# Optimization experiments

Measured on AMD Instinct MI355X. Metric: run time of the kernel, lower is better.

The kernel has to match this reference:

```python
import jax, jax.numpy as jnp
import numpy as np

B, T, D = 16, 4096, 256
CODEBOOK_SIZE = 1024
COMMITMENT = 1.0


def setup_inputs() -> dict:
    key = jax.random.key(0)
    kx, kc = jax.random.split(key)
    x = jax.random.normal(kx, (B, T, D), dtype=jnp.float32)
    codebook = jax.random.normal(kc, (CODEBOOK_SIZE, D), dtype=jnp.float32)
    return {"x": x, "codebook": codebook}


def reference(x, codebook):
    # x: [B, T, D] continuous latents; codebook: [K, D]
    flat = x.reshape(-1, x.shape[-1])  # [N, D]
    # does not affect argmin but is kept for faithfulness to torch.cdist-style math)
    x_sq = jnp.sum(flat * flat, axis=1, keepdims=True)            # [N, 1]
    c_sq = jnp.sum(codebook * codebook, axis=1)                   # [K]
    dist = x_sq - 2.0 * (flat @ codebook.T) + c_sq[None, :]       # [N, K]
    indices = jnp.argmin(dist, axis=1)                            # [N] int
    quantized = codebook[indices].reshape(x.shape)                # gather, [B, T, D]
    # commitment loss: encoder pulled toward (stopped) codes
    commit_loss = COMMITMENT * jnp.mean(
        (x - jax.lax.stop_gradient(quantized)) ** 2
    )
    # straight-through estimator
    out = x + jax.lax.stop_gradient(quantized - x)
    return out, indices.reshape(x.shape[:-1]), commit_loss
```

## Files before the change

### kernel.cpp

```cpp
#include <hip/hip_runtime.h>

#define N_TOK 65536
#define DIM   256
#define KCODE 1024

#define NTHREADS 256
#define TM 128
#define TN 128
#define BK 32
#define NCHUNK 8
#define NSTAGE 24

#define REFINE_EPS 0.125f
#define TIE_THETA 1.0e-4

#define WS_CSQ_OFF   16
#define WS_IDX_OFF   2048
#define WS_PAIRS_OFF (WS_IDX_OFF + N_TOK)
#define WS_CBPK_OFF  (WS_PAIRS_OFF + N_TOK * NCHUNK * 4)

typedef float f32x4  __attribute__((ext_vector_type(4)));
typedef short bf16x8 __attribute__((ext_vector_type(8)));
typedef short s16x8  __attribute__((ext_vector_type(8)));

__global__ void zero_loss_kernel(float* ws) {
    if (threadIdx.x == 0) ws[0] = 0.0f;
}

__global__ void rowsq_np_kernel(const float* __restrict__ m,
                                float* __restrict__ out, int rows) {
#pragma clang fp contract(off)
    int row = blockIdx.x * 16 + (threadIdx.x >> 4);
    int l   = threadIdx.x & 15;
    if (row >= rows) return;
    int h = l >> 3;
    int j = l & 7;
    const float* p = m + (size_t)row * DIM + h * 128 + j;
    float v = p[0];
    float r = v * v;
#pragma unroll
    for (int i = 1; i < 16; ++i) {
        float w  = p[i * 8];
        float w2 = w * w;
        r = r + w2;
    }
    float t = r + __shfl_xor(r, 1);
    t = t + __shfl_xor(t, 2);
    t = t + __shfl_xor(t, 4);
    t = t + __shfl_xor(t, 8);
    if (l == 0) out[row] = t;
}

__device__ __forceinline__ void ins2(float d, int idx,
                                     float& d1, int& i1, float& d2, int& i2) {
    if (d < d1 || (d == d1 && idx < i1)) {
        d2 = d1; i2 = i1; d1 = d; i1 = idx;
    } else if ((d < d2 || (d == d2 && idx < i2)) && idx != i1) {
        d2 = d; i2 = idx;
    }
}

__device__ __forceinline__ void f2bf_split(float v, short& hi, short& lo) {
    unsigned u = __float_as_uint(v);
    unsigned r = (u + 0x7fffu + ((u >> 16) & 1u)) >> 16;
    hi = (short)r;
    float hf = __uint_as_float(r << 16);
    float lf = v - hf;
    unsigned u2 = __float_as_uint(lf);
    unsigned r2 = (u2 + 0x7fffu + ((u2 >> 16) & 1u)) >> 16;
    lo = (short)r2;
}

__global__ void pack_tiles_kernel(const float* __restrict__ src,
                                  unsigned short* __restrict__ dst,
                                  int total) {
    int tid = blockIdx.x * blockDim.x + threadIdx.x;
    if (tid >= total) return;
    int s   = tid & 3;
    int r   = (tid >> 2) & 127;
    int kc  = (tid >> 9) & 7;
    int g   = tid >> 12;
    int oct = s ^ ((r >> 1) & 3);

    const float4* xr = reinterpret_cast<const float4*>(
        src + ((size_t)(g * 128 + r)) * DIM + kc * 32 + oct * 8);
    float4 v0 = xr[0];
    float4 v1 = xr[1];

    float f[8] = {v0.x, v0.y, v0.z, v0.w, v1.x, v1.y, v1.z, v1.w};
    s16x8 hv, lv;
#pragma unroll
    for (int i = 0; i < 8; ++i) {
        short h, l;
        f2bf_split(f[i], h, l);
        hv[i] = h; lv[i] = l;
    }
    size_t base_hi = (((size_t)(g * 16 + kc) * 128 + r) << 5) + s * 8;
    size_t base_lo = (((size_t)(g * 16 + 8 + kc) * 128 + r) << 5) + s * 8;
    *reinterpret_cast<s16x8*>(dst + base_hi) = hv;
    *reinterpret_cast<s16x8*>(dst + base_lo) = lv;
}

__device__ __forceinline__ void gload_lds16(const unsigned short* g, unsigned short* lds) {
    __builtin_amdgcn_global_load_lds(
        (const __attribute__((address_space(1))) unsigned int*)g,
        (__attribute__((address_space(3))) unsigned int*)lds, 16, 0, 0);
}

__launch_bounds__(NTHREADS, 5)
__global__ void vq_main_kernel(const unsigned short* __restrict__ xpk,
                               const unsigned short* __restrict__ cbpk,
                               const float* __restrict__ csq,
                               float4* __restrict__ pairs) {
    __shared__ __align__(16) unsigned short shbuf[2][2 * TM * BK];

    const int tid  = threadIdx.x;
    const int w    = tid >> 6;
    const int wy   = w >> 1;
    const int wx   = w & 1;
    const int lane = tid & 63;
    const int lm   = lane & 15;
    const int q    = lane >> 4;

    const int bx     = blockIdx.x;
    const int jj     = bx >> 3;
    const int grp    = (bx & 7) + ((jj >> 3) << 3);
    const int cchunk = jj & 7;
    const int tok0   = grp * TM;
    const int code0  = cchunk * TN;

    float cs_reg[4];
#pragma unroll
    for (int ni = 0; ni < 4; ++ni)
        cs_reg[ni] = csq[code0 + wx * 64 + ni * 16 + lm];

    f32x4 acc[4][4];
#pragma unroll
    for (int mi = 0; mi < 4; ++mi)
#pragma unroll
        for (int ni = 0; ni < 4; ++ni)
            acc[mi][ni] = (f32x4){0.f, 0.f, 0.f, 0.f};

    int offA[4], offB[4];
#pragma unroll
    for (int mi = 0; mi < 4; ++mi) {
        int r = wy * 64 + mi * 16 + lm;
        offA[mi] = r * BK + ((q ^ ((r >> 1) & 3)) * 8);
    }
#pragma unroll
    for (int ni = 0; ni < 4; ++ni) {
        int r = wx * 64 + ni * 16 + lm;
        offB[ni] = TM * BK + r * BK + ((q ^ ((r >> 1) & 3)) * 8);
    }

    const int lsrc = w * 1024 + lane * 8;
    auto stage = [&](int p, int s) {
        const int seg = s >> 3;
        const int kc  = s & 7;
        const int pa  = (seg == 2) ? 8 : 0;
        const int pb  = (seg == 1) ? 8 : 0;
        const unsigned short* ga = xpk  + (((size_t)(grp    * 16 + pa + kc)) << 12) + lsrc;
        const unsigned short* gb = cbpk + (((size_t)(cchunk * 16 + pb + kc)) << 12) + lsrc;
        unsigned short* At = &shbuf[p][w * 1024];
        unsigned short* Bt = &shbuf[p][TM * BK + w * 1024];
        gload_lds16(ga,       At);
        gload_lds16(ga + 512, At + 512);
        gload_lds16(gb,       Bt);
        gload_lds16(gb + 512, Bt + 512);
    };

    stage(0, 0);
    __syncthreads();

    int p = 0;
#pragma unroll 1
    for (int s = 0; s < NSTAGE; ++s) {
        if (s < NSTAGE - 1) stage(p ^ 1, s + 1);

        const unsigned short* buf = &shbuf[p][0];
        bf16x8 af[4], bf[4];
#pragma unroll
        for (int mi = 0; mi < 4; ++mi)
            af[mi] = *reinterpret_cast<const bf16x8*>(buf + offA[mi]);
#pragma unroll
        for (int ni = 0; ni < 4; ++ni)
            bf[ni] = *reinterpret_cast<const bf16x8*>(buf + offB[ni]);
#pragma unroll
        for (int mi = 0; mi < 4; ++mi)
#pragma unroll
            for (int ni = 0; ni < 4; ++ni)
                acc[mi][ni] = __builtin_amdgcn_mfma_f32_16x16x32_bf16(
                    af[mi], bf[ni], acc[mi][ni], 0, 0, 0);

        __syncthreads();
        p ^= 1;
    }

    float4 (*pairs_sh)[2] = reinterpret_cast<float4(*)[2]>(&shbuf[0][0]);

#pragma unroll
    for (int mi = 0; mi < 4; ++mi) {
#pragma unroll
        for (int r = 0; r < 4; ++r) {
            int row_local = wy * 64 + mi * 16 + q * 4 + r;
            float l1 = 3.4e38f, l2 = 3.4e38f;
            int   j1 = 0x7fffffff, j2 = 0x7fffffff;
#pragma unroll
            for (int ni = 0; ni < 4; ++ni) {
                float d = cs_reg[ni] - 2.0f * acc[mi][ni][r];
                ins2(d, code0 + wx * 64 + ni * 16 + lm, l1, j1, l2, j2);
            }
#pragma unroll
            for (int m = 1; m < 16; m <<= 1) {
                float o1 = __shfl_xor(l1, m);
                int   p1 = __shfl_xor(j1, m);
                float o2 = __shfl_xor(l2, m);
                int   p2 = __shfl_xor(j2, m);
                ins2(o1, p1, l1, j1, l2, j2);
                ins2(o2, p2, l1, j1, l2, j2);
            }
            if (lm == 0) {
                float4 pr;
                pr.x = l1; pr.y = l2;
                pr.z = __int_as_float(j1); pr.w = __int_as_float(j2);
                pairs_sh[row_local][wx] = pr;
            }
        }
    }
    __syncthreads();
    if (tid < TM) {
        float4 pa = pairs_sh[tid][0];
        float4 pb = pairs_sh[tid][1];
        float d1 = pa.x, d2 = pa.y;
        int   i1 = __float_as_int(pa.z), i2 = __float_as_int(pa.w);
        ins2(pb.x, __float_as_int(pb.z), d1, i1, d2, i2);
        ins2(pb.y, __float_as_int(pb.w), d1, i1, d2, i2);
        float4 pr;
        pr.x = d1; pr.y = d2;
        pr.z = __int_as_float(i1); pr.w = __int_as_float(i2);
        pairs[(size_t)(tok0 + tid) * NCHUNK + cchunk] = pr;
    }
}

__global__ void merge_refine_kernel(const float* __restrict__ x,
                                    const float* __restrict__ cb,
                                    const float4* __restrict__ pairs,
                                    int* __restrict__ idx_out) {
    int t = blockIdx.x * 256 + threadIdx.x;
    if (t >= N_TOK) return;
    float4 p0 = pairs[(size_t)t * NCHUNK];
    float d1 = p0.x, d2 = p0.y;
    int   i1 = __float_as_int(p0.z), i2 = __float_as_int(p0.w);
#pragma unroll
    for (int c = 1; c < NCHUNK; ++c) {
        float4 p = pairs[(size_t)t * NCHUNK + c];
        ins2(p.x, __float_as_int(p.z), d1, i1, d2, i2);
        ins2(p.y, __float_as_int(p.w), d1, i1, d2, i2);
    }

    int pick = i1;
    if (d2 - d1 < REFINE_EPS) {
        const float* xr = x + (size_t)t * DIM;
        const float* c1 = cb + (size_t)i1 * DIM;
        const float* c2 = cb + (size_t)i2 * DIM;
        double sA = 0.0, dA = 0.0, sB = 0.0, dB = 0.0;
        for (int k = 0; k < DIM; ++k) {
            double xv = (double)xr[k];
            double a  = (double)c1[k];
            double b  = (double)c2[k];
            sA += a * a; dA += xv * a;
            sB += b * b; dB += xv * b;
        }
        double DA  = sA - 2.0 * dA;
        double DB  = sB - 2.0 * dB;
        double gap = DB - DA;
        if (gap > TIE_THETA)       pick = i1;
        else if (gap < -TIE_THETA) pick = i2;
        else                       pick = (i1 < i2) ? i1 : i2;
    }
    idx_out[t] = pick;
}

__launch_bounds__(NTHREADS)
__global__ void output_kernel(const float* __restrict__ x,
                              const float* __restrict__ cb,
                              const int* __restrict__ idx,
                              float* __restrict__ out_q,
                              float* __restrict__ out_idx,
                              float* __restrict__ loss_ws) {
    __shared__ int   sh_idx[TM];
    __shared__ float wsum[4];
    const int tid  = threadIdx.x;
    const int tok0 = blockIdx.x * TM;

    if (tid < TM) sh_idx[tid] = idx[tok0 + tid];
    __syncthreads();

    float lsum = 0.0f;
    for (int t = 0; t < TM; ++t) {
        int code = sh_idx[t];
        float qv = cb[(size_t)code * DIM + tid];
        float xv = x[(size_t)(tok0 + t) * DIM + tid];
        out_q[(size_t)(tok0 + t) * DIM + tid] = xv + (qv - xv);
        float df = xv - qv;
        lsum = fmaf(df, df, lsum);
    }
    if (tid < TM) out_idx[tok0 + tid] = (float)sh_idx[tid];

#pragma unroll
    for (int off = 1; off < 64; off <<= 1) lsum += __shfl_xor(lsum, off);
    if ((tid & 63) == 0) wsum[tid >> 6] = lsum;
    __syncthreads();
    if (tid == 0) atomicAdd(loss_ws, (wsum[0] + wsum[1]) + (wsum[2] + wsum[3]));
}

__global__ void finalize_kernel(const float* ws, float* out_loss) {
    if (threadIdx.x == 0) out_loss[0] = ws[0] * (1.0f / 16777216.0f);
}

extern "C" void kernel_launch(void* const* d_in, const int* in_sizes, int n_in,
                              void* d_out, int out_size, void* d_ws, size_t ws_size,
                              hipStream_t stream) {
    const float* x  = (const float*)d_in[0];
    const float* cb = (const float*)d_in[1];

    float* out      = (float*)d_out;
    float* out_q    = out;
    float* out_idx  = out + (size_t)N_TOK * DIM;
    float* out_loss = out_idx + N_TOK;

    float*  ws    = (float*)d_ws;
    float*  csq   = ws + WS_CSQ_OFF;
    int*    idx   = (int*)(ws + WS_IDX_OFF);
    float4* pairs = (float4*)(ws + WS_PAIRS_OFF);
    unsigned short* cbpk = (unsigned short*)(ws + WS_CBPK_OFF);
    unsigned short* xpk  = (unsigned short*)out_q;

    zero_loss_kernel<<<1, 64, 0, stream>>>(ws);
    rowsq_np_kernel<<<KCODE / 16, 256, 0, stream>>>(cb, csq, KCODE);
    pack_tiles_kernel<<<(N_TOK * 32) / 256, 256, 0, stream>>>(x, xpk, N_TOK * 32);
    pack_tiles_kernel<<<(KCODE * 32) / 256, 256, 0, stream>>>(cb, cbpk, KCODE * 32);
    vq_main_kernel<<<(N_TOK / TM) * NCHUNK, NTHREADS, 0, stream>>>(xpk, cbpk, csq, pairs);
    merge_refine_kernel<<<N_TOK / 256, 256, 0, stream>>>(x, cb, pairs, idx);
    output_kernel<<<N_TOK / TM, NTHREADS, 0, stream>>>(x, cb, idx, out_q, out_idx, ws);
    finalize_kernel<<<1, 64, 0, stream>>>(ws, out_loss);
}
```

Measured before the change: 803.3 us.

## Triple-buffer GEMM loads, fuse merge into output kernel, drop zero kernel

The main distance kernel now keeps three LDS buffers with two stages in flight, using an explicit vmcnt wait plus barrier instead of __syncthreads, and raises MFMA priority with setprio. The merge/refine step is folded into the output kernel, and the pairs layout is transposed to chunk-major so the merge reads are coalesced. The loss-zeroing kernel is merged into the row-norm kernel. These changes cut launch count and global round trips and aim to hide load latency, at the cost of more LDS per block and lower declared occupancy (launch bound 3 instead of 5).

New measurement: 816.4 us. About the same (+1.6%).

```diff
diff --git a/kernel.cpp b/kernel.cpp
--- a/kernel.cpp
+++ b/kernel.cpp
@@ -10,6 +10,7 @@
 #define BK 32
 #define NCHUNK 8
 #define NSTAGE 24
+#define OTM 128
 
 #define REFINE_EPS 0.125f
 #define TIE_THETA 1.0e-4
@@ -23,13 +24,11 @@
 typedef short bf16x8 __attribute__((ext_vector_type(8)));
 typedef short s16x8  __attribute__((ext_vector_type(8)));
 
-__global__ void zero_loss_kernel(float* ws) {
-    if (threadIdx.x == 0) ws[0] = 0.0f;
-}
-
 __global__ void rowsq_np_kernel(const float* __restrict__ m,
-                                float* __restrict__ out, int rows) {
+                                float* __restrict__ out,
+                                float* __restrict__ loss_ws, int rows) {
 #pragma clang fp contract(off)
+    if (blockIdx.x == 0 && threadIdx.x == 0) loss_ws[0] = 0.0f;
     int row = blockIdx.x * 16 + (threadIdx.x >> 4);
     int l   = threadIdx.x & 15;
     if (row >= rows) return;
@@ -107,12 +106,13 @@
         (__attribute__((address_space(3))) unsigned int*)lds, 16, 0, 0);
 }
 
-__launch_bounds__(NTHREADS, 5)
+__launch_bounds__(NTHREADS, 3)
 __global__ void vq_main_kernel(const unsigned short* __restrict__ xpk,
                                const unsigned short* __restrict__ cbpk,
                                const float* __restrict__ csq,
                                float4* __restrict__ pairs) {
-    __shared__ __align__(16) unsigned short shbuf[2][2 * TM * BK];
+    __shared__ __align__(16) unsigned short shbuf[3][2 * TM * BK];
+    __shared__ float4 pairs_sh[TM][2];
 
     const int tid  = threadIdx.x;
     const int w    = tid >> 6;
@@ -170,14 +170,21 @@
     };
 
     stage(0, 0);
-    __syncthreads();
-
-    int p = 0;
+    stage(1, 1);
+
+    int pc = 0;
 #pragma unroll 1
-    for (int s = 0; s < NSTAGE; ++s) {
-        if (s < NSTAGE - 1) stage(p ^ 1, s + 1);
-
-        const unsigned short* buf = &shbuf[p][0];
+    for (int s = 0; s < NSTAGE - 1; ++s) {
+        asm volatile("s_waitcnt vmcnt(4)" ::: "memory");
+        __builtin_amdgcn_s_barrier();
+        __builtin_amdgcn_sched_barrier(0);
+
+        if (s + 2 < NSTAGE) {
+            int pn = pc + 2; if (pn >= 3) pn -= 3;
+            stage(pn, s + 2);
+        }
+
+        const unsigned short* buf = &shbuf[pc][0];
         bf16x8 af[4], bf[4];
 #pragma unroll
         for (int mi = 0; mi < 4; ++mi)
@@ -185,18 +192,40 @@
 #pragma unroll
         for (int ni = 0; ni < 4; ++ni)
             bf[ni] = *reinterpret_cast<const bf16x8*>(buf + offB[ni]);
+
+        __builtin_amdgcn_s_setprio(1);
 #pragma unroll
         for (int mi = 0; mi < 4; ++mi)
 #pragma unroll
             for (int ni = 0; ni < 4; ++ni)
                 acc[mi][ni] = __builtin_amdgcn_mfma_f32_16x16x32_bf16(
                     af[mi], bf[ni], acc[mi][ni], 0, 0, 0);
-
-        __syncthreads();
-        p ^= 1;
-    }
-
-    float4 (*pairs_sh)[2] = reinterpret_cast<float4(*)[2]>(&shbuf[0][0]);
+        __builtin_amdgcn_s_setprio(0);
+
+        pc = (pc == 2) ? 0 : pc + 1;
+    }
+
+    asm volatile("s_waitcnt vmcnt(0)" ::: "memory");
+    __builtin_amdgcn_s_barrier();
+    __builtin_amdgcn_sched_barrier(0);
+    {
+        const unsigned short* buf = &shbuf[pc][0];
+        bf16x8 af[4], bf[4];
+#pragma unroll
+        for (int mi = 0; mi < 4; ++mi)
+            af[mi] = *reinterpret_cast<const bf16x8*>(buf + offA[mi]);
+#pragma unroll
+        for (int ni = 0; ni < 4; ++ni)
+            bf[ni] = *reinterpret_cast<const bf16x8*>(buf + offB[ni]);
+        __builtin_amdgcn_s_setprio(1);
+#pragma unroll
+        for (int mi = 0; mi < 4; ++mi)
+#pragma unroll
+            for (int ni = 0; ni < 4; ++ni)
+                acc[mi][ni] = __builtin_amdgcn_mfma_f32_16x16x32_bf16(
+                    af[mi], bf[ni], acc[mi][ni], 0, 0, 0);
+        __builtin_amdgcn_s_setprio(0);
+    }
 
 #pragma unroll
     for (int mi = 0; mi < 4; ++mi) {
@@ -238,66 +267,61 @@
         float4 pr;
         pr.x = d1; pr.y = d2;
         pr.z = __int_as_float(i1); pr.w = __int_as_float(i2);
-        pairs[(size_t)(tok0 + tid) * NCHUNK + cchunk] = pr;
-    }
-}
-
-__global__ void merge_refine_kernel(const float* __restrict__ x,
+        pairs[(size_t)cchunk * N_TOK + tok0 + tid] = pr;
+    }
+}
+
+__launch_bounds__(256)
+__global__ void merge_output_kernel(const float* __restrict__ x,
                                     const float* __restrict__ cb,
                                     const float4* __restrict__ pairs,
-                                    int* __restrict__ idx_out) {
-    int t = blockIdx.x * 256 + threadIdx.x;
-    if (t >= N_TOK) return;
-    float4 p0 = pairs[(size_t)t * NCHUNK];
-    float d1 = p0.x, d2 = p0.y;
-    int   i1 = __float_as_int(p0.z), i2 = __float_as_int(p0.w);
-#pragma unroll
-    for (int c = 1; c < NCHUNK; ++c) {
-        float4 p = pairs[(size_t)t * NCHUNK + c];
-        ins2(p.x, __float_as_int(p.z), d1, i1, d2, i2);
-        ins2(p.y, __float_as_int(p.w), d1, i1, d2, i2);
-    }
-
-    int pick = i1;
-    if (d2 - d1 < REFINE_EPS) {
-        const float* xr = x + (size_t)t * DIM;
-        const float* c1 = cb + (size_t)i1 * DIM;
-        const float* c2 = cb + (size_t)i2 * DIM;
-        double sA = 0.0, dA = 0.0, sB = 0.0, dB = 0.0;
-        for (int k = 0; k < DIM; ++k) {
-            double xv = (double)xr[k];
-            double a  = (double)c1[k];
-            double b  = (double)c2[k];
-            sA += a * a; dA += xv * a;
-            sB += b * b; dB += xv * b;
-        }
-        double DA  = sA - 2.0 * dA;
-        double DB  = sB - 2.0 * dB;
-        double gap = DB - DA;
-        if (gap > TIE_THETA)       pick = i1;
-        else if (gap < -TIE_THETA) pick = i2;
-        else                       pick = (i1 < i2) ? i1 : i2;
-    }
-    idx_out[t] = pick;
-}
-
-__launch_bounds__(NTHREADS)
-__global__ void output_kernel(const float* __restrict__ x,
-                              const float* __restrict__ cb,
-                              const int* __restrict__ idx,
-                              float* __restrict__ out_q,
-                              float* __restrict__ out_idx,
-                              float* __restrict__ loss_ws) {
-    __shared__ int   sh_idx[TM];
+                                    float* __restrict__ out_q,
+                                    float* __restrict__ out_idx,
+                                    float* __restrict__ loss_ws) {
+    __shared__ int   sh_idx[OTM];
     __shared__ float wsum[4];
     const int tid  = threadIdx.x;
-    const int tok0 = blockIdx.x * TM;
-
-    if (tid < TM) sh_idx[tid] = idx[tok0 + tid];
+    const int tok0 = blockIdx.x * OTM;
+
+    if (tid < OTM) {
+        const int t = tok0 + tid;
+        float4 p0 = pairs[t];
+        float d1 = p0.x, d2 = p0.y;
+        int   i1 = __float_as_int(p0.z), i2 = __float_as_int(p0.w);
+#pragma unroll
+        for (int c = 1; c < NCHUNK; ++c) {
+            float4 p = pairs[(size_t)c * N_TOK + t];
+            ins2(p.x, __float_as_int(p.z), d1, i1, d2, i2);
+            ins2(p.y, __float_as_int(p.w), d1, i1, d2, i2);
+        }
+
+        int pick = i1;
+        if (d2 - d1 < REFINE_EPS) {
+            const float* xr = x + (size_t)t * DIM;
+            const float* c1 = cb + (size_t)i1 * DIM;
+            const float* c2 = cb + (size_t)i2 * DIM;
+            double sA = 0.0, dA = 0.0, sB = 0.0, dB = 0.0;
+            for (int k = 0; k < DIM; ++k) {
+                double xv = (double)xr[k];
+                double a  = (double)c1[k];
+                double b  = (double)c2[k];
+                sA += a * a; dA += xv * a;
+                sB += b * b; dB += xv * b;
+            }
+            double DA  = sA - 2.0 * dA;
+            double DB  = sB - 2.0 * dB;
+            double gap = DB - DA;
+            if (gap > TIE_THETA)       pick = i1;
+            else if (gap < -TIE_THETA) pick = i2;
+            else                       pick = (i1 < i2) ? i1 : i2;
+        }
+        sh_idx[tid] = pick;
+        out_idx[t]  = (float)pick;
+    }
     __syncthreads();
 
     float lsum = 0.0f;
-    for (int t = 0; t < TM; ++t) {
+    for (int t = 0; t < OTM; ++t) {
         int code = sh_idx[t];
         float qv = cb[(size_t)code * DIM + tid];
         float xv = x[(size_t)(tok0 + t) * DIM + tid];
@@ -305,7 +329,6 @@
         float df = xv - qv;
         lsum = fmaf(df, df, lsum);
     }
-    if (tid < TM) out_idx[tok0 + tid] = (float)sh_idx[tid];
 
 #pragma unroll
     for (int off = 1; off < 64; off <<= 1) lsum += __shfl_xor(lsum, off);
@@ -331,17 +354,14 @@
 
     float*  ws    = (float*)d_ws;
     float*  csq   = ws + WS_CSQ_OFF;
-    int*    idx   = (int*)(ws + WS_IDX_OFF);
     float4* pairs = (float4*)(ws + WS_PAIRS_OFF);
     unsigned short* cbpk = (unsigned short*)(ws + WS_CBPK_OFF);
     unsigned short* xpk  = (unsigned short*)out_q;
 
-    zero_loss_kernel<<<1, 64, 0, stream>>>(ws);
-    rowsq_np_kernel<<<KCODE / 16, 256, 0, stream>>>(cb, csq, KCODE);
+    rowsq_np_kernel<<<KCODE / 16, 256, 0, stream>>>(cb, csq, ws, KCODE);
     pack_tiles_kernel<<<(N_TOK * 32) / 256, 256, 0, stream>>>(x, xpk, N_TOK * 32);
     pack_tiles_kernel<<<(KCODE * 32) / 256, 256, 0, stream>>>(cb, cbpk, KCODE * 32);
     vq_main_kernel<<<(N_TOK / TM) * NCHUNK, NTHREADS, 0, stream>>>(xpk, cbpk, csq, pairs);
-    merge_refine_kernel<<<N_TOK / 256, 256, 0, stream>>>(x, cb, pairs, idx);
-    output_kernel<<<N_TOK / TM, NTHREADS, 0, stream>>>(x, cb, idx, out_q, out_idx, ws);
+    merge_output_kernel<<<N_TOK / OTM, 256, 0, stream>>>(x, cb, pairs, out_q, out_idx, ws);
     finalize_kernel<<<1, 64, 0, stream>>>(ws, out_loss);
 }
```
